# Performance work log

Hardware: AMD Instinct MI355X
Metric: run time of the kernel (lower is better)

Reference implementation:

```python
import jax, jax.numpy as jnp
import numpy as np
from jax import lax

B, V, E = 8, 1024, 32          # batch, nodes, raw node-embedding dim
F, H = 64, 4                   # node_encoding, num_heads
HID = 64                       # encoder/decoder hidden size
LAYERS = 2                     # graph_layers
FLOW_ITERS = 10
BIG = 1e9
COST_C = 1.0                   # quadratic cost: c*x^2, inv_derivative(y)=y/(2c)
DEG_P = 16.0 / V               # ~16 avg out-degree


def setup_inputs() -> dict:
    key = jax.random.key(0)
    ks = jax.random.split(key, 24)
    demands = jax.random.normal(ks[0], (B, V, 1), jnp.float32)
    demands = demands - jnp.mean(demands, axis=1, keepdims=True)  # balanced supply/demand
    node_embeddings = jax.random.normal(ks[1], (V, E), jnp.float32)
    adj = (jax.random.uniform(ks[2], (V, V)) < DEG_P).astype(jnp.float32)
    adj = jnp.maximum(adj, jnp.eye(V, dtype=jnp.float32))  # ensure nonempty rows
    s = 0.05
    p = lambda k, shp: jax.random.normal(k, shp, jnp.float32) * s
    return {
        'demands': demands, 'node_embeddings': node_embeddings, 'adj': adj,
        'enc_w1': p(ks[3], (E + 1, HID)), 'enc_b1': jnp.zeros((HID,), jnp.float32),
        'enc_w2': p(ks[4], (HID, F)),     'enc_b2': jnp.zeros((F,), jnp.float32),
        'gat_w':  p(ks[5], (H, F, F)),
        'gat_a1': p(ks[6], (H, F)), 'gat_a2': p(ks[7], (H, F)),
        'gate_w': p(ks[8], (F, F)), 'gate_u': p(ks[9], (F, F)),
        'gate_b': jnp.zeros((F,), jnp.float32),
        'dec_w1': p(ks[10], (F, HID)), 'dec_b1': jnp.zeros((HID,), jnp.float32),
        'dec_w2': p(ks[11], (HID, V)), 'dec_b2': jnp.zeros((V,), jnp.float32),
        'dual_w1': p(ks[12], (F, HID)), 'dual_b1': jnp.zeros((HID,), jnp.float32),
        'dual_w2': p(ks[13], (HID, 1)), 'dual_b2': jnp.zeros((1,), jnp.float32),
    }


def _forward(demands, node_embeddings, adj,
             enc_w1, enc_b1, enc_w2, enc_b2,
             gat_w, gat_a1, gat_a2,
             gate_w, gate_u, gate_b,
             dec_w1, dec_b1, dec_w2, dec_b2,
             dual_w1, dual_b1, dual_w2, dual_b2):
    node_bias = -BIG * (1.0 - adj)                     # [V, V]
    # ---- encoder MLP (relu hidden) ----
    x = jnp.broadcast_to(node_embeddings[None], (B, V, E))
    x = jnp.concatenate([x, demands], axis=2)          # [B, V, E+1]
    enc = jax.nn.relu(x @ enc_w1 + enc_b1) @ enc_w2 + enc_b2   # [B, V, F]
    enc = jax.nn.relu(enc)
    # ---- GAT + gate, shared weights across graph_layers ----
    for _ in range(LAYERS):
        t = jnp.einsum('bvf,hfg->bhvg', enc, gat_w)            # [B, H, V, F]
        s_self = jnp.einsum('bhvg,hg->bhv', t, gat_a1)
        s_nbr = jnp.einsum('bhvg,hg->bhv', t, gat_a2)
        logits = jax.nn.leaky_relu(s_self[..., :, None] + s_nbr[..., None, :], 0.2)
        coefs = jax.nn.softmax(logits + node_bias[None, None], axis=-1)  # [B,H,V,V]
        heads = jnp.einsum('bhvw,bhwg->bhvg', coefs, t)
        nxt = jax.nn.relu(jnp.mean(heads, axis=1))             # [B, V, F]
        z = jax.nn.sigmoid(nxt @ gate_w + enc @ gate_u + gate_b)
        enc = z * nxt + (1.0 - z) * enc
    # ---- decoder -> masked softmax flow weights ----
    pred = (enc @ dec_w1 + dec_b1) @ dec_w2 + dec_b2           # [B, V, V] (linear MLP)
    pred = jnp.square(pred)
    flow_weights = jax.nn.softmax(pred + node_bias[None], axis=-1)
    # ---- iterative min-cost-flow solve ----
    def flow_step(flow, _):
        inflow = jnp.sum(flow, axis=1)[:, :, None]             # [B, V, 1]
        return flow_weights * jax.nn.relu(inflow - demands), None
    flow, _ = lax.scan(flow_step, jnp.zeros_like(flow_weights), None, length=FLOW_ITERS)[0], None
    flow = lax.scan(flow_step, jnp.zeros_like(flow_weights), None, length=FLOW_ITERS)[0]
    flow_cost = jnp.sum(COST_C * jnp.square(flow), axis=(1, 2))  # [B]
    # ---- dual variables / dual cost ----
    dv = (enc @ dual_w1 + dual_b1) @ dual_w2 + dual_b2         # [B, V, 1]
    dual_diff = dv - jnp.swapaxes(dv, 1, 2)                    # [B, V, V]
    dual_flows = adj[None] * jax.nn.relu(dual_diff / (2.0 * COST_C))
    dual_flow_cost = COST_C * jnp.square(dual_flows) - dual_diff * dual_flows
    dual_demand = jnp.sum(dv * demands, axis=(1, 2))
    dual_cost = jnp.sum(dual_flow_cost, axis=(1, 2)) - dual_demand
    loss = jnp.mean(flow_cost - dual_cost)
    return loss


def reference(demands, node_embeddings, adj,
              enc_w1, enc_b1, enc_w2, enc_b2,
              gat_w, gat_a1, gat_a2,
              gate_w, gate_u, gate_b,
              dec_w1, dec_b1, dec_w2, dec_b2,
              dual_w1, dual_b1, dual_w2, dual_b2):
    return _forward(demands, node_embeddings, adj,
                    enc_w1, enc_b1, enc_w2, enc_b2,
                    gat_w, gat_a1, gat_a2,
                    gate_w, gate_u, gate_b,
                    dec_w1, dec_b1, dec_w2, dec_b2,
                    dual_w1, dual_b1, dual_w2, dual_b2)
```

## Files before the change

kernel.cpp:

```cpp
#include <hip/hip_runtime.h>
#include <math.h>

#define B 8
#define V 1024
#define E 32
#define H 4
#define HIDN 64
#define CAP 64
#define MAXNNZ 20480
#define SE (MAXNNZ / V)
#define ZBLK 128


__device__ __forceinline__ float wave_sum(float v) {
  for (int o = 32; o > 0; o >>= 1) v += __shfl_xor(v, o);
  return v;
}
__device__ __forceinline__ float wave_max(float v) {
  for (int o = 32; o > 0; o >>= 1) v = fmaxf(v, __shfl_xor(v, o));
  return v;
}

__global__ void zero_kernel(int* __restrict__ deg_in) {
  int t = blockIdx.x * 256 + threadIdx.x;
  if (t < V) deg_in[t] = 0;
}

#define ENV 8
__global__ void setup_kernel(const float* __restrict__ adj, const float* __restrict__ demands,
                             const float* __restrict__ emb,
                             const float* __restrict__ ew1, const float* __restrict__ eb1,
                             const float* __restrict__ ew2, const float* __restrict__ eb2,
                             const float* __restrict__ dec_w2,
                             int* __restrict__ nbr, int* __restrict__ deg,
                             int* __restrict__ deg_in, float* __restrict__ enc,
                             float* __restrict__ w2t, float* __restrict__ fwe,
                             unsigned int* __restrict__ meta) {
  int blk = blockIdx.x;
  int j = threadIdx.x;
  if (blk < V) {
    int v = blk;
    int base = 0;
    for (int c = 0; c < V; c += 64) {
      float a = adj[v * V + c + j];
      unsigned long long m = __ballot(a > 0.5f);
      int pos = __popcll(m & ((1ull << j) - 1ull));
      if (a > 0.5f && base + pos < CAP) {
        nbr[v * CAP + base + pos] = c + j;
        atomicAdd(&deg_in[c + j], 1);
      }
      base += __popcll(m);
    }
    if (j == 0) deg[v] = (base < CAP) ? base : CAP;
  } else if (blk < 2 * V) {
    int eb = blk - V;
    int b = eb & 7;
    int v0 = (eb >> 3) * ENV;
    int bv0 = b * V + v0;
    __shared__ float xs[ENV][E + 1];
    __shared__ float hs[ENV][64];
#pragma unroll
    for (int n = 0; n < ENV; ++n) {
      if (j < E) xs[n][j] = emb[(v0 + n) * E + j];
      else if (j == E) xs[n][E] = demands[b * V + v0 + n];
    }
    __syncthreads();
    float h[ENV];
#pragma unroll
    for (int n = 0; n < ENV; ++n) h[n] = eb1[j];
    for (int i = 0; i < E + 1; ++i) {
      float wv = ew1[i * 64 + j];
#pragma unroll
      for (int n = 0; n < ENV; ++n) h[n] += xs[n][i] * wv;
    }
#pragma unroll
    for (int n = 0; n < ENV; ++n) hs[n][j] = fmaxf(h[n], 0.f);
    __syncthreads();
    float o[ENV];
#pragma unroll
    for (int n = 0; n < ENV; ++n) o[n] = eb2[j];
    for (int i = 0; i < 64; ++i) {
      float wv = ew2[i * 64 + j];
#pragma unroll
      for (int n = 0; n < ENV; ++n) o[n] += hs[n][i] * wv;
    }
#pragma unroll
    for (int n = 0; n < ENV; ++n) enc[(bv0 + n) * 64 + j] = fmaxf(o[n], 0.f);
  } else if (blk < 3 * V) {
    int w = blk - 2 * V;
    w2t[w * 64 + j] = dec_w2[j * V + w];
  } else {
    int idx = (blk - 3 * V) * 64 + j;
    for (int i = idx; i < B * MAXNNZ; i += ZBLK * 64) fwe[i] = 0.f;
    for (int i = idx; i < MAXNNZ; i += ZBLK * 64) meta[i] = 0u;
  }
}

__global__ void scan_kernel(const int* __restrict__ deg_in, int* __restrict__ in_off) {
  int lane = threadIdx.x;
  int vals[16];
  int tot = 0;
#pragma unroll
  for (int i = 0; i < 16; ++i) {
    vals[i] = tot;
    tot += deg_in[lane * 16 + i];
  }
  int run = tot;
  for (int o = 1; o < 64; o <<= 1) {
    int u = __shfl_up(run, o);
    if (lane >= o) run += u;
  }
  int excl = run - tot;
#pragma unroll
  for (int i = 0; i < 16; ++i) in_off[lane * 16 + i] = excl + vals[i];
  if (lane == 63) in_off[V] = excl + tot;
}

__global__ void csc_fill(const int* __restrict__ nbr, const int* __restrict__ deg,
                         int* __restrict__ deg_in, const int* __restrict__ in_off,
                         int* __restrict__ csc_pos) {
  int v = blockIdx.x, k = threadIdx.x;
  if (k < deg[v]) {
    int w = nbr[v * CAP + k];
    int old = atomicSub(&deg_in[w], 1);
    csc_pos[v * CAP + k] = in_off[w] + old - 1;
  }
}

#define TNV 8
__global__ void t_kernel(const float* __restrict__ enc, const float* __restrict__ gat_w,
                         const float* __restrict__ a1, const float* __restrict__ a2,
                         float* __restrict__ t, float* __restrict__ s_self,
                         float* __restrict__ s_nbr) {
  int b = blockIdx.x & 7;
  int v0 = (blockIdx.x >> 3) * TNV;
  int bv0 = b * V + v0;
  int tid = threadIdx.x;
  int h = tid >> 6, g = tid & 63;
  __shared__ float es[TNV][64];
  for (int i = tid; i < TNV * 64; i += 256) es[i >> 6][i & 63] = enc[bv0 * 64 + i];
  __syncthreads();
  float acc[TNV];
#pragma unroll
  for (int n = 0; n < TNV; ++n) acc[n] = 0.f;
  const float* w = gat_w + h * 64 * 64 + g;
  for (int f = 0; f < 64; ++f) {
    float wf = w[f * 64];
#pragma unroll
    for (int n = 0; n < TNV; ++n) acc[n] += es[n][f] * wf;
  }
  float a1v = a1[h * 64 + g], a2v = a2[h * 64 + g];
#pragma unroll
  for (int n = 0; n < TNV; ++n) {
    t[((size_t)(b * H + h) * V + (v0 + n)) * 64 + g] = acc[n];
    float v1 = wave_sum(acc[n] * a1v);
    float v2 = wave_sum(acc[n] * a2v);
    if (g == 0) {
      s_self[(b * H + h) * V + (v0 + n)] = v1;
      s_nbr[(b * H + h) * V + (v0 + n)] = v2;
    }
  }
}

__global__ void gat_kernel(const float* __restrict__ enc_in, const float* __restrict__ t,
                           const float* __restrict__ s_self, const float* __restrict__ s_nbr,
                           const int* __restrict__ nbr, const int* __restrict__ deg,
                           const float* __restrict__ gate_w, const float* __restrict__ gate_u,
                           const float* __restrict__ gate_b, float* __restrict__ enc_out) {
  int b = blockIdx.x & 7;
  int v = blockIdx.x >> 3;
  int bv = b * V + v;
  int tid = threadIdx.x;
  int h = tid >> 6, lane = tid & 63;
  int dvv = deg[v];
  int wk = (lane < dvv) ? nbr[v * CAP + lane] : 0;
  float logit = -1e30f;
  if (lane < dvv) {
    float x = s_self[(b * H + h) * V + v] + s_nbr[(b * H + h) * V + wk];
    logit = (x > 0.f) ? x : 0.2f * x;
  }
  float m = wave_max(logit);
  float e = (lane < dvv) ? __expf(logit - m) : 0.f;
  float s = wave_sum(e);
  float coef = e / s;
  const float* tb = t + (size_t)(b * H + h) * (V * 64);
  float acc = 0.f;
  for (int k = 0; k < dvv; ++k) {
    float c = __shfl(coef, k);
    int w = __shfl(wk, k);
    acc += c * tb[w * 64 + lane];
  }
  __shared__ float hsum[4][64];
  __shared__ float nxts[64], encs[64];
  hsum[h][lane] = acc;
  __syncthreads();
  if (tid < 64) {
    float s4 = hsum[0][tid] + hsum[1][tid] + hsum[2][tid] + hsum[3][tid];
    nxts[tid] = fmaxf(0.25f * s4, 0.f);
    encs[tid] = enc_in[bv * 64 + tid];
  }
  __syncthreads();
  float part = 0.f;
  for (int f = h * 16; f < h * 16 + 16; ++f)
    part += nxts[f] * gate_w[f * 64 + lane] + encs[f] * gate_u[f * 64 + lane];
  __syncthreads();
  hsum[h][lane] = part;
  __syncthreads();
  if (tid < 64) {
    float zs = hsum[0][tid] + hsum[1][tid] + hsum[2][tid] + hsum[3][tid] + gate_b[tid];
    float z = 1.f / (1.f + __expf(-zs));
    enc_out[bv * 64 + tid] = z * nxts[tid] + (1.f - z) * encs[tid];
  }
}

#define DNV 8
__global__ void dec_dual_kernel(const float* __restrict__ enc, const float* __restrict__ dw1,
                                const float* __restrict__ db1, const float* __restrict__ uw1,
                                const float* __restrict__ ub1, const float* __restrict__ uw2,
                                const float* __restrict__ ub2, float* __restrict__ hid,
                                float* __restrict__ dv) {
  int b = blockIdx.x & 7;
  int v0 = (blockIdx.x >> 3) * DNV;
  int bv0 = b * V + v0;
  int j = threadIdx.x;
  __shared__ float es[DNV][64];
#pragma unroll
  for (int n = 0; n < DNV; ++n) es[n][j] = enc[(bv0 + n) * 64 + j];
  __syncthreads();
  float hj[DNV], uj[DNV];
#pragma unroll
  for (int n = 0; n < DNV; ++n) { hj[n] = db1[j]; uj[n] = ub1[j]; }
  for (int f = 0; f < 64; ++f) {
    float a = dw1[f * 64 + j], c = uw1[f * 64 + j];
#pragma unroll
    for (int n = 0; n < DNV; ++n) {
      hj[n] += es[n][f] * a;
      uj[n] += es[n][f] * c;
    }
  }
  float w2v = uw2[j];
#pragma unroll
  for (int n = 0; n < DNV; ++n) {
    hid[(bv0 + n) * 64 + j] = hj[n];
    float s = wave_sum(uj[n] * w2v);
    if (j == 0) dv[bv0 + n] = s + ub2[0];
  }
}

__global__ void fw_kernel(const float* __restrict__ hid, const float* __restrict__ w2t,
                          const float* __restrict__ b2, const int* __restrict__ nbr,
                          const int* __restrict__ deg, const int* __restrict__ csc_pos,
                          float* __restrict__ fwe, unsigned int* __restrict__ meta,
                          float* __restrict__ rssq) {
  int b = blockIdx.x & 7;
  int v = blockIdx.x >> 3;
  int bv = b * V + v;
  int k = threadIdx.x;
  __shared__ float hs[64];
  hs[k] = hid[bv * 64 + k];
  __syncthreads();
  int dvv = deg[v];
  int w = (k < dvv) ? nbr[v * CAP + k] : 0;
  const float4* wrow = (const float4*)(w2t + w * 64);
  const float4* hv4 = (const float4*)hs;
  float d = 0.f;
#pragma unroll
  for (int f = 0; f < 16; ++f) {
    float4 wv = wrow[f];
    float4 hv = hv4[f];
    d += hv.x * wv.x + hv.y * wv.y + hv.z * wv.z + hv.w * wv.w;
  }
  d += b2[w];
  float pp = d * d;
  float myp = (k < dvv) ? pp : -1e30f;
  float m = wave_max(myp);
  float e = (k < dvv) ? __expf(myp - m) : 0.f;
  float s = wave_sum(e);
  float coef = e / s;
  if (k < dvv) {
    int idx = csc_pos[v * CAP + k];
    fwe[(size_t)b * MAXNNZ + idx] = coef;
    meta[idx] = (unsigned)v | ((unsigned)w << 16);
  }
  float r = wave_sum(coef * coef);
  if (k == 0) rssq[bv] = r;
}

__global__ __launch_bounds__(1024) void flow_dual_kernel(
    const float* __restrict__ fwe, const unsigned int* __restrict__ meta,
    const float* __restrict__ rssq, const float* __restrict__ dv,
    const float* __restrict__ demands, const int* __restrict__ nbr_out,
    const int* __restrict__ deg_out, float* __restrict__ partial) {
  int b = blockIdx.x;
  int v = threadIdx.x;
  __shared__ float o[V], infl[V], dvs[V];
  __shared__ float red[16];
  float dem = demands[b * V + v];
  dvs[v] = dv[b * V + v];
  o[v] = fmaxf(-dem, 0.f);
  infl[v] = 0.f;
  const float4* fp = (const float4*)(fwe + (size_t)b * MAXNNZ + v * SE);
  const uint4* mp = (const uint4*)(meta + v * SE);
  float fr[SE];
  unsigned mr[SE];
#pragma unroll
  for (int i = 0; i < SE / 4; ++i) {
    float4 f4 = fp[i];
    uint4 m4 = mp[i];
    fr[4 * i + 0] = f4.x; fr[4 * i + 1] = f4.y; fr[4 * i + 2] = f4.z; fr[4 * i + 3] = f4.w;
    mr[4 * i + 0] = m4.x; mr[4 * i + 1] = m4.y; mr[4 * i + 2] = m4.z; mr[4 * i + 3] = m4.w;
  }
  __syncthreads();
  for (int it = 0; it < 9; ++it) {
    float acc = 0.f;
    int pdst = -1;
#pragma unroll
    for (int i = 0; i < SE; ++i) {
      int src = mr[i] & 0xFFFF;
      int dst = mr[i] >> 16;
      if (dst != pdst) {
        if (acc != 0.f) atomicAdd(&infl[pdst], acc);
        acc = 0.f;
        pdst = dst;
      }
      acc += fr[i] * o[src];
    }
    if (acc != 0.f) atomicAdd(&infl[pdst], acc);
    __syncthreads();
    float nv = fmaxf(infl[v] - dem, 0.f);
    o[v] = nv;
    infl[v] = 0.f;
    __syncthreads();
  }
  float o10 = o[v];
  float local = o10 * o10 * rssq[b * V + v];
  float dvv = dvs[v];
  int dout = deg_out[v];
  float acc = 0.f;
  for (int k = 0; k < dout; ++k) {
    float diff = dvv - dvs[nbr_out[v * CAP + k]];
    if (diff > 0.f) acc += diff * diff;
  }
  local += 0.25f * acc + dvv * dem;
  local = wave_sum(local);
  if ((v & 63) == 0) red[v >> 6] = local;
  __syncthreads();
  if (v < 16) {
    float r = red[v];
    for (int o2 = 8; o2 > 0; o2 >>= 1) r += __shfl_xor(r, o2, 16);
    if (v == 0) partial[b] = r;
  }
}

__global__ void final_kernel(const float* __restrict__ partial, float* __restrict__ out) {
  if (threadIdx.x == 0) {
    float s = 0.f;
    for (int b = 0; b < B; ++b) s += partial[b];
    out[0] = s * (1.0f / B);
  }
}

extern "C" void kernel_launch(void* const* d_in, const int* in_sizes, int n_in,
                              void* d_out, int out_size, void* d_ws, size_t ws_size,
                              hipStream_t stream) {
  const float* demands = (const float*)d_in[0];
  const float* emb     = (const float*)d_in[1];
  const float* adj     = (const float*)d_in[2];
  const float* enc_w1  = (const float*)d_in[3];
  const float* enc_b1  = (const float*)d_in[4];
  const float* enc_w2  = (const float*)d_in[5];
  const float* enc_b2  = (const float*)d_in[6];
  const float* gat_w   = (const float*)d_in[7];
  const float* gat_a1  = (const float*)d_in[8];
  const float* gat_a2  = (const float*)d_in[9];
  const float* gate_w  = (const float*)d_in[10];
  const float* gate_u  = (const float*)d_in[11];
  const float* gate_b  = (const float*)d_in[12];
  const float* dec_w1  = (const float*)d_in[13];
  const float* dec_b1  = (const float*)d_in[14];
  const float* dec_w2  = (const float*)d_in[15];
  const float* dec_b2  = (const float*)d_in[16];
  const float* dual_w1 = (const float*)d_in[17];
  const float* dual_b1 = (const float*)d_in[18];
  const float* dual_w2 = (const float*)d_in[19];
  const float* dual_b2 = (const float*)d_in[20];

  char* p = (char*)d_ws;
  auto alloc = [&](size_t n) { void* r = (void*)p; p += (n + 255) & ~(size_t)255; return r; };
  int* nbr_out   = (int*)alloc((size_t)V * CAP * 4);
  int* deg_out   = (int*)alloc((size_t)V * 4);
  int* deg_in    = (int*)alloc((size_t)V * 4);
  int* in_off    = (int*)alloc((size_t)(V + 1) * 4);
  int* csc_pos   = (int*)alloc((size_t)V * CAP * 4);
  float* fwe     = (float*)alloc((size_t)B * MAXNNZ * 4);
  unsigned int* meta = (unsigned int*)alloc((size_t)MAXNNZ * 4);
  float* w2t     = (float*)alloc((size_t)HIDN * V * 4);
  float* encA    = (float*)alloc((size_t)B * V * 64 * 4);
  float* encB    = (float*)alloc((size_t)B * V * 64 * 4);
  float* t       = (float*)alloc((size_t)B * H * V * 64 * 4);
  float* s_self  = (float*)alloc((size_t)B * H * V * 4);
  float* s_nbr   = (float*)alloc((size_t)B * H * V * 4);
  float* hid     = (float*)alloc((size_t)B * V * 64 * 4);
  float* dv      = (float*)alloc((size_t)B * V * 4);
  float* rssq    = (float*)alloc((size_t)B * V * 4);
  float* partial = (float*)alloc((size_t)B * 4);

  zero_kernel<<<V / 256, 256, 0, stream>>>(deg_in);
  setup_kernel<<<3 * V + ZBLK, 64, 0, stream>>>(adj, demands, emb, enc_w1, enc_b1, enc_w2,
                                                enc_b2, dec_w2, nbr_out, deg_out, deg_in,
                                                encA, w2t, fwe, meta);
  scan_kernel<<<1, 64, 0, stream>>>(deg_in, in_off);
  csc_fill<<<V, 64, 0, stream>>>(nbr_out, deg_out, deg_in, in_off, csc_pos);
  float* cur = encA;
  float* nxt = encB;
  for (int l = 0; l < 2; ++l) {
    t_kernel<<<B * V / TNV, 256, 0, stream>>>(cur, gat_w, gat_a1, gat_a2, t, s_self, s_nbr);
    gat_kernel<<<B * V, 256, 0, stream>>>(cur, t, s_self, s_nbr, nbr_out, deg_out,
                                          gate_w, gate_u, gate_b, nxt);
    float* tmp = cur; cur = nxt; nxt = tmp;
  }
  dec_dual_kernel<<<B * V / DNV, 64, 0, stream>>>(cur, dec_w1, dec_b1, dual_w1, dual_b1,
                                                  dual_w2, dual_b2, hid, dv);
  fw_kernel<<<B * V, 64, 0, stream>>>(hid, w2t, dec_b2, nbr_out, deg_out, csc_pos,
                                      fwe, meta, rssq);
  flow_dual_kernel<<<B, 1024, 0, stream>>>(fwe, meta, rssq, dv, demands, nbr_out, deg_out,
                                           partial);
  final_kernel<<<1, 64, 0, stream>>>(partial, (float*)d_out);
}
```

Measured before the change: 170.6 us.

## Reassociate GAT attention to aggregate before projection and fuse layer kernels

Precomputes W·a1 and W·a2 so the attention scores come straight from the encodings, and computes them in the setup kernel and at the end of each layer. Neighbour embeddings are aggregated with the softmax coefficients first and then projected through W per head. This removes the large per-head t buffer and the separate t_kernel launch. Each block now handles 8 nodes, which amortises the gate-weight loads but adds more barriers and shared memory per block.

```diff
diff --git a/kernel.cpp b/kernel.cpp
--- a/kernel.cpp
+++ b/kernel.cpp
@@ -21,9 +21,23 @@
   return v;
 }
 
-__global__ void zero_kernel(int* __restrict__ deg_in) {
-  int t = blockIdx.x * 256 + threadIdx.x;
-  if (t < V) deg_in[t] = 0;
+__global__ void zero_wa_kernel(int* __restrict__ deg_in, const float* __restrict__ gat_w,
+                               const float* __restrict__ a1, const float* __restrict__ a2,
+                               float* __restrict__ wa1, float* __restrict__ wa2) {
+  if (blockIdx.x < 4) {
+    deg_in[blockIdx.x * 256 + threadIdx.x] = 0;
+  } else {
+    int h = threadIdx.x >> 6, f = threadIdx.x & 63;
+    float s1 = 0.f, s2 = 0.f;
+    const float* W = gat_w + h * 4096 + f * 64;
+    for (int g = 0; g < 64; ++g) {
+      float w = W[g];
+      s1 += w * a1[h * 64 + g];
+      s2 += w * a2[h * 64 + g];
+    }
+    wa1[h * 64 + f] = s1;
+    wa2[h * 64 + f] = s2;
+  }
 }
 
 #define ENV 8
@@ -32,8 +46,10 @@
                              const float* __restrict__ ew1, const float* __restrict__ eb1,
                              const float* __restrict__ ew2, const float* __restrict__ eb2,
                              const float* __restrict__ dec_w2,
+                             const float* __restrict__ wa1, const float* __restrict__ wa2,
                              int* __restrict__ nbr, int* __restrict__ deg,
                              int* __restrict__ deg_in, float* __restrict__ enc,
+                             float* __restrict__ ss, float* __restrict__ sn,
                              float* __restrict__ w2t, float* __restrict__ fwe,
                              unsigned int* __restrict__ meta) {
   int blk = blockIdx.x;
@@ -85,7 +101,22 @@
       for (int n = 0; n < ENV; ++n) o[n] += hs[n][i] * wv;
     }
 #pragma unroll
-    for (int n = 0; n < ENV; ++n) enc[(bv0 + n) * 64 + j] = fmaxf(o[n], 0.f);
+    for (int n = 0; n < ENV; ++n) {
+      o[n] = fmaxf(o[n], 0.f);
+      enc[(bv0 + n) * 64 + j] = o[n];
+    }
+#pragma unroll
+    for (int n = 0; n < ENV; ++n) {
+#pragma unroll
+      for (int hh = 0; hh < H; ++hh) {
+        float v1 = wave_sum(o[n] * wa1[hh * 64 + j]);
+        float v2 = wave_sum(o[n] * wa2[hh * 64 + j]);
+        if (j == 0) {
+          ss[(b * H + hh) * V + v0 + n] = v1;
+          sn[(b * H + hh) * V + v0 + n] = v2;
+        }
+      }
+    }
   } else if (blk < 3 * V) {
     int w = blk - 2 * V;
     w2t[w * 64 + j] = dec_w2[j * V + w];
@@ -127,89 +158,110 @@
   }
 }
 
-#define TNV 8
-__global__ void t_kernel(const float* __restrict__ enc, const float* __restrict__ gat_w,
-                         const float* __restrict__ a1, const float* __restrict__ a2,
-                         float* __restrict__ t, float* __restrict__ s_self,
-                         float* __restrict__ s_nbr) {
+#define GNV 8
+__global__ __launch_bounds__(256) void gat2_kernel(
+    const float* __restrict__ enc_in, const float* __restrict__ ss_in,
+    const float* __restrict__ sn_in, const int* __restrict__ nbr,
+    const int* __restrict__ deg, const float* __restrict__ gat_w,
+    const float* __restrict__ gate_w, const float* __restrict__ gate_u,
+    const float* __restrict__ gate_b, const float* __restrict__ wa1,
+    const float* __restrict__ wa2, float* __restrict__ enc_out,
+    float* __restrict__ ss_out, float* __restrict__ sn_out, int write_s) {
   int b = blockIdx.x & 7;
-  int v0 = (blockIdx.x >> 3) * TNV;
-  int bv0 = b * V + v0;
+  int v0 = (blockIdx.x >> 3) * GNV;
   int tid = threadIdx.x;
-  int h = tid >> 6, g = tid & 63;
-  __shared__ float es[TNV][64];
-  for (int i = tid; i < TNV * 64; i += 256) es[i >> 6][i & 63] = enc[bv0 * 64 + i];
-  __syncthreads();
-  float acc[TNV];
-#pragma unroll
-  for (int n = 0; n < TNV; ++n) acc[n] = 0.f;
-  const float* w = gat_w + h * 64 * 64 + g;
-  for (int f = 0; f < 64; ++f) {
-    float wf = w[f * 64];
-#pragma unroll
-    for (int n = 0; n < TNV; ++n) acc[n] += es[n][f] * wf;
-  }
-  float a1v = a1[h * 64 + g], a2v = a2[h * 64 + g];
-#pragma unroll
-  for (int n = 0; n < TNV; ++n) {
-    t[((size_t)(b * H + h) * V + (v0 + n)) * 64 + g] = acc[n];
-    float v1 = wave_sum(acc[n] * a1v);
-    float v2 = wave_sum(acc[n] * a2v);
-    if (g == 0) {
-      s_self[(b * H + h) * V + (v0 + n)] = v1;
-      s_nbr[(b * H + h) * V + (v0 + n)] = v2;
-    }
-  }
-}
-
-__global__ void gat_kernel(const float* __restrict__ enc_in, const float* __restrict__ t,
-                           const float* __restrict__ s_self, const float* __restrict__ s_nbr,
-                           const int* __restrict__ nbr, const int* __restrict__ deg,
-                           const float* __restrict__ gate_w, const float* __restrict__ gate_u,
-                           const float* __restrict__ gate_b, float* __restrict__ enc_out) {
-  int b = blockIdx.x & 7;
-  int v = blockIdx.x >> 3;
-  int bv = b * V + v;
-  int tid = threadIdx.x;
-  int h = tid >> 6, lane = tid & 63;
-  int dvv = deg[v];
-  int wk = (lane < dvv) ? nbr[v * CAP + lane] : 0;
-  float logit = -1e30f;
-  if (lane < dvv) {
-    float x = s_self[(b * H + h) * V + v] + s_nbr[(b * H + h) * V + wk];
-    logit = (x > 0.f) ? x : 0.2f * x;
-  }
-  float m = wave_max(logit);
-  float e = (lane < dvv) ? __expf(logit - m) : 0.f;
-  float s = wave_sum(e);
-  float coef = e / s;
-  const float* tb = t + (size_t)(b * H + h) * (V * 64);
-  float acc = 0.f;
-  for (int k = 0; k < dvv; ++k) {
-    float c = __shfl(coef, k);
-    int w = __shfl(wk, k);
-    acc += c * tb[w * 64 + lane];
-  }
-  __shared__ float hsum[4][64];
-  __shared__ float nxts[64], encs[64];
-  hsum[h][lane] = acc;
-  __syncthreads();
-  if (tid < 64) {
-    float s4 = hsum[0][tid] + hsum[1][tid] + hsum[2][tid] + hsum[3][tid];
-    nxts[tid] = fmaxf(0.25f * s4, 0.f);
-    encs[tid] = enc_in[bv * 64 + tid];
-  }
-  __syncthreads();
-  float part = 0.f;
-  for (int f = h * 16; f < h * 16 + 16; ++f)
-    part += nxts[f] * gate_w[f * 64 + lane] + encs[f] * gate_u[f * 64 + lane];
-  __syncthreads();
-  hsum[h][lane] = part;
-  __syncthreads();
-  if (tid < 64) {
-    float zs = hsum[0][tid] + hsum[1][tid] + hsum[2][tid] + hsum[3][tid] + gate_b[tid];
+  int wid = tid >> 6, lane = tid & 63;
+  __shared__ float agg[GNV][H][64];
+  __shared__ float gpart[GNV][4][64];
+  __shared__ float nxts[GNV][64];
+  __shared__ float encs[GNV][64];
+  const float* eb = enc_in + (size_t)b * V * 64;
+  for (int i = tid; i < GNV * 64; i += 256) encs[i >> 6][i & 63] = eb[v0 * 64 + i];
+  for (int n = wid; n < GNV; n += 4) {
+    int v = v0 + n;
+    int dvv = deg[v];
+    int wk = (lane < dvv) ? nbr[v * CAP + lane] : 0;
+    float c[H];
+#pragma unroll
+    for (int h = 0; h < H; ++h) {
+      float x = ss_in[(b * H + h) * V + v] + sn_in[(b * H + h) * V + wk];
+      x = (x > 0.f) ? x : 0.2f * x;
+      if (lane >= dvv) x = -1e30f;
+      float m = wave_max(x);
+      float e = (lane < dvv) ? __expf(x - m) : 0.f;
+      float s = wave_sum(e);
+      c[h] = e / s;
+    }
+    float a0 = 0.f, a1v = 0.f, a2v = 0.f, a3v = 0.f;
+    for (int k = 0; k < dvv; ++k) {
+      int w = __shfl(wk, k);
+      float ev = eb[w * 64 + lane];
+      a0 += __shfl(c[0], k) * ev;
+      a1v += __shfl(c[1], k) * ev;
+      a2v += __shfl(c[2], k) * ev;
+      a3v += __shfl(c[3], k) * ev;
+    }
+    agg[n][0][lane] = a0;
+    agg[n][1][lane] = a1v;
+    agg[n][2][lane] = a2v;
+    agg[n][3][lane] = a3v;
+  }
+  __syncthreads();
+  {
+    const float* W = gat_w + wid * 4096;
+    float hv[GNV];
+#pragma unroll
+    for (int n = 0; n < GNV; ++n) hv[n] = 0.f;
+    for (int f = 0; f < 64; ++f) {
+      float wf = W[f * 64 + lane];
+#pragma unroll
+      for (int n = 0; n < GNV; ++n) hv[n] += agg[n][wid][f] * wf;
+    }
+#pragma unroll
+    for (int n = 0; n < GNV; ++n) gpart[n][wid][lane] = hv[n];
+  }
+  __syncthreads();
+  for (int i = tid; i < GNV * 64; i += 256) {
+    int n = i >> 6, g = i & 63;
+    float s4 = gpart[n][0][g] + gpart[n][1][g] + gpart[n][2][g] + gpart[n][3][g];
+    nxts[n][g] = fmaxf(0.25f * s4, 0.f);
+  }
+  __syncthreads();
+  {
+    float part[GNV];
+#pragma unroll
+    for (int n = 0; n < GNV; ++n) part[n] = 0.f;
+    for (int f = wid * 16; f < wid * 16 + 16; ++f) {
+      float gw = gate_w[f * 64 + lane], gu = gate_u[f * 64 + lane];
+#pragma unroll
+      for (int n = 0; n < GNV; ++n) part[n] += nxts[n][f] * gw + encs[n][f] * gu;
+    }
+    __syncthreads();
+#pragma unroll
+    for (int n = 0; n < GNV; ++n) gpart[n][wid][lane] = part[n];
+  }
+  __syncthreads();
+  for (int i = tid; i < GNV * 64; i += 256) {
+    int n = i >> 6, g = i & 63;
+    float zs = gpart[n][0][g] + gpart[n][1][g] + gpart[n][2][g] + gpart[n][3][g] + gate_b[g];
     float z = 1.f / (1.f + __expf(-zs));
-    enc_out[bv * 64 + tid] = z * nxts[tid] + (1.f - z) * encs[tid];
+    float out = z * nxts[n][g] + (1.f - z) * encs[n][g];
+    encs[n][g] = out;
+    enc_out[((size_t)b * V + v0 + n) * 64 + g] = out;
+  }
+  if (write_s) {
+    __syncthreads();
+    float w1v = wa1[wid * 64 + lane], w2v = wa2[wid * 64 + lane];
+#pragma unroll
+    for (int n = 0; n < GNV; ++n) {
+      float e = encs[n][lane];
+      float ssv = wave_sum(e * w1v);
+      float snv = wave_sum(e * w2v);
+      if (lane == 0) {
+        ss_out[(b * H + wid) * V + v0 + n] = ssv;
+        sn_out[(b * H + wid) * V + v0 + n] = snv;
+      }
+    }
   }
 }
 
@@ -395,31 +447,32 @@
   float* fwe     = (float*)alloc((size_t)B * MAXNNZ * 4);
   unsigned int* meta = (unsigned int*)alloc((size_t)MAXNNZ * 4);
   float* w2t     = (float*)alloc((size_t)HIDN * V * 4);
+  float* wa1     = (float*)alloc((size_t)H * 64 * 4);
+  float* wa2     = (float*)alloc((size_t)H * 64 * 4);
   float* encA    = (float*)alloc((size_t)B * V * 64 * 4);
   float* encB    = (float*)alloc((size_t)B * V * 64 * 4);
-  float* t       = (float*)alloc((size_t)B * H * V * 64 * 4);
-  float* s_self  = (float*)alloc((size_t)B * H * V * 4);
-  float* s_nbr   = (float*)alloc((size_t)B * H * V * 4);
+  float* ssA     = (float*)alloc((size_t)B * H * V * 4);
+  float* snA     = (float*)alloc((size_t)B * H * V * 4);
+  float* ssB     = (float*)alloc((size_t)B * H * V * 4);
+  float* snB     = (float*)alloc((size_t)B * H * V * 4);
   float* hid     = (float*)alloc((size_t)B * V * 64 * 4);
   float* dv      = (float*)alloc((size_t)B * V * 4);
   float* rssq    = (float*)alloc((size_t)B * V * 4);
   float* partial = (float*)alloc((size_t)B * 4);
 
-  zero_kernel<<<V / 256, 256, 0, stream>>>(deg_in);
-  setup_kernel<<<3 * V + ZBLK, 64, 0, stream>>>(adj, demands, emb, enc_w1, enc_b1, enc_w2,
-                                                enc_b2, dec_w2, nbr_out, deg_out, deg_in,
-                                                encA, w2t, fwe, meta);
+  zero_wa_kernel<<<5, 256, 0, stream>>>(deg_in, gat_w, gat_a1, gat_a2, wa1, wa2);
+  setup_kernel<<<3 * V + ZBLK, 64, 0, stream>>>(
+      adj, demands, emb, enc_w1, enc_b1, enc_w2, enc_b2, dec_w2, wa1, wa2,
+      nbr_out, deg_out, deg_in, encA, ssA, snA, w2t, fwe, meta);
   scan_kernel<<<1, 64, 0, stream>>>(deg_in, in_off);
   csc_fill<<<V, 64, 0, stream>>>(nbr_out, deg_out, deg_in, in_off, csc_pos);
-  float* cur = encA;
-  float* nxt = encB;
-  for (int l = 0; l < 2; ++l) {
-    t_kernel<<<B * V / TNV, 256, 0, stream>>>(cur, gat_w, gat_a1, gat_a2, t, s_self, s_nbr);
-    gat_kernel<<<B * V, 256, 0, stream>>>(cur, t, s_self, s_nbr, nbr_out, deg_out,
-                                          gate_w, gate_u, gate_b, nxt);
-    float* tmp = cur; cur = nxt; nxt = tmp;
-  }
-  dec_dual_kernel<<<B * V / DNV, 64, 0, stream>>>(cur, dec_w1, dec_b1, dual_w1, dual_b1,
+  gat2_kernel<<<B * V / GNV, 256, 0, stream>>>(encA, ssA, snA, nbr_out, deg_out, gat_w,
+                                               gate_w, gate_u, gate_b, wa1, wa2,
+                                               encB, ssB, snB, 1);
+  gat2_kernel<<<B * V / GNV, 256, 0, stream>>>(encB, ssB, snB, nbr_out, deg_out, gat_w,
+                                               gate_w, gate_u, gate_b, wa1, wa2,
+                                               encA, ssA, snA, 0);
+  dec_dual_kernel<<<B * V / DNV, 64, 0, stream>>>(encA, dec_w1, dec_b1, dual_w1, dual_b1,
                                                   dual_w2, dual_b2, hid, dv);
   fw_kernel<<<B * V, 64, 0, stream>>>(hid, w2t, dec_b2, nbr_out, deg_out, csc_pos,
                                       fwe, meta, rssq);
```

Measured after the change: 150.9 us. -11.5%, faster.
